# Performance work log

Hardware: AMD Instinct MI355X
Metric: run time of the kernel (lower is better)

The kernel has to match this reference:

```python
import jax, jax.numpy as jnp
import numpy as np

N = 20000      # nodes
E = 320000     # edges
DIN = 128
DOUT = 10
H = 1024
HM = 256
EPS = 1e-5


def setup_inputs() -> dict:
    key = jax.random.key(0)
    ks = jax.random.split(key, 16)
    sc = 0.02
    return {
        "x": jax.random.normal(ks[0], (N, DIN), dtype=jnp.float32),
        "edge_index": jax.random.randint(ks[1], (2, E), 0, N, dtype=jnp.int64),
        "edge_weight": jax.random.uniform(ks[2], (E,), dtype=jnp.float32),
        "W1": jax.random.normal(ks[3], (DIN, H), dtype=jnp.float32) * sc,
        "b1": jnp.zeros((H,), jnp.float32),
        "g1": jnp.ones((H,), jnp.float32),
        "beta1": jnp.zeros((H,), jnp.float32),
        "W2": jax.random.normal(ks[4], (H, H), dtype=jnp.float32) * sc,
        "b2": jnp.zeros((H,), jnp.float32),
        "g2": jnp.ones((H,), jnp.float32),
        "beta2": jnp.zeros((H,), jnp.float32),
        "Wl1": jax.random.normal(ks[5], (H, HM), dtype=jnp.float32) * sc,
        "bl1": jnp.zeros((HM,), jnp.float32),
        "Wl2": jax.random.normal(ks[6], (HM, DOUT), dtype=jnp.float32) * sc,
        "bl2": jnp.zeros((DOUT,), jnp.float32),
    }


def _gcn_conv(x, W, b, src, dst, w):
    # PyG GCNConv: linear transform, symmetric normalization (self-loops
    # already appended to src/dst/w), scatter-add aggregation at dst.
    h = x @ W                                        # [N, out]
    deg = jax.ops.segment_sum(w, dst, num_segments=N)
    dinv = jnp.where(deg > 0, jax.lax.rsqrt(deg), 0.0)
    norm = dinv[src] * w * dinv[dst]                 # [E+N]
    agg = jax.ops.segment_sum(norm[:, None] * h[src], dst, num_segments=N)
    return agg + b


def _batchnorm(x, g, b):
    m = x.mean(axis=0)
    v = jnp.mean(jnp.square(x - m), axis=0)          # biased var (torch BN)
    return g * (x - m) * jax.lax.rsqrt(v + EPS) + b


def reference(x, edge_index, edge_weight,
              W1, b1, g1, beta1, W2, b2, g2, beta2,
              Wl1, bl1, Wl2, bl2):
    loop = jnp.arange(N, dtype=edge_index.dtype)
    src = jnp.concatenate([edge_index[0], loop])
    dst = jnp.concatenate([edge_index[1], loop])
    w = jnp.concatenate([edge_weight, jnp.ones((N,), edge_weight.dtype)])

    h = jax.nn.relu(_batchnorm(_gcn_conv(x, W1, b1, src, dst, w), g1, beta1))
    h = jax.nn.relu(_batchnorm(_gcn_conv(h, W2, b2, src, dst, w), g2, beta2))
    h = jax.nn.relu(h @ Wl1 + bl1) @ Wl2 + bl2
    return jax.nn.log_softmax(h, axis=1)
```

## Files before the change

### kernel.cpp

```cpp
#include <hip/hip_runtime.h>
#include <math.h>

static constexpr int Nn  = 20000;
static constexpr int Ne  = 320000;
static constexpr int DIN = 128;
static constexpr int DOUTc = 10;
static constexpr int Hc  = 1024;
static constexpr int HMc = 256;
static constexpr float EPSc = 1e-5f;
static constexpr int NB_SCAN = (Nn + 255) / 256;

typedef __bf16 bf16_t;
typedef __bf16 bf16x8 __attribute__((ext_vector_type(8)));
typedef __bf16 bf16x4 __attribute__((ext_vector_type(4)));
typedef float  f32x4  __attribute__((ext_vector_type(4)));

__device__ __forceinline__ void gload_lds16(const bf16_t* g, bf16_t* lds) {
    __builtin_amdgcn_global_load_lds(
        (const __attribute__((address_space(1))) void*)g,
        (__attribute__((address_space(3))) void*)lds, 16, 0, 0);
}

__global__ __launch_bounds__(256)
void deg_init_k(float* __restrict__ deg, int* __restrict__ cnt, float* __restrict__ stats)
{
    int i = blockIdx.x * 256 + threadIdx.x;
    if (i < Nn) { deg[i] = 1.0f; cnt[i] = 0; }
    if (i < 4 * Hc) stats[i] = 0.f;
}

__global__ __launch_bounds__(256)
void deg_edge_k(const float* __restrict__ w, const int* __restrict__ dstv,
                float* __restrict__ deg, int* __restrict__ cnt) {
    int e = blockIdx.x * 256 + threadIdx.x;
    if (e < Ne) {
        int d = dstv[e];
        atomicAdd(&deg[d], w[e]);
        atomicAdd(&cnt[d], 1);
    }
}

__global__ __launch_bounds__(256)
void scanA_k(const int* __restrict__ cnt, int* __restrict__ row_ptr, int* __restrict__ blk,
             float* __restrict__ deg)
{
    __shared__ int wsum[4];
    int b = blockIdx.x, tid = threadIdx.x, lane = tid & 63, wv = tid >> 6;
    int i = b * 256 + tid;
    if (i < Nn) deg[i] = rsqrtf(deg[i]);
    int v = (i < Nn) ? cnt[i] : 0;
    int s = v;
    #pragma unroll
    for (int off = 1; off < 64; off <<= 1) {
        int t = __shfl_up(s, off, 64);
        if (lane >= off) s += t;
    }
    if (lane == 63) wsum[wv] = s;
    __syncthreads();
    int wo = 0;
    #pragma unroll
    for (int k = 0; k < 4; ++k) if (k < wv) wo += wsum[k];
    if (i < Nn) row_ptr[i] = wo + s - v;
    if (tid == 255) blk[b] = wo + s;
}

__global__ __launch_bounds__(128)
void scanB_k(int* __restrict__ blk)
{
    __shared__ int w0;
    int tid = threadIdx.x, lane = tid & 63, wv = tid >> 6;
    int v = (tid < NB_SCAN) ? blk[tid] : 0;
    int s = v;
    #pragma unroll
    for (int off = 1; off < 64; off <<= 1) {
        int t = __shfl_up(s, off, 64);
        if (lane >= off) s += t;
    }
    if (tid == 63) w0 = s;
    __syncthreads();
    int excl = s - v + (wv ? w0 : 0);
    if (tid < NB_SCAN) blk[tid] = excl;
}

__global__ __launch_bounds__(256)
void scanC_k(int* __restrict__ row_ptr, const int* __restrict__ blk, int* __restrict__ cursor)
{
    int b = blockIdx.x;
    int i = b * 256 + threadIdx.x;
    if (i < Nn) {
        int r = row_ptr[i] + blk[b];
        row_ptr[i] = r;
        cursor[i]  = r;
    }
    if (i == 0) row_ptr[Nn] = Ne;
}

__global__ __launch_bounds__(256)
void csr_fill_k(const int* __restrict__ srcv, const int* __restrict__ dstv,
                const float* __restrict__ w, const float* __restrict__ dinv,
                int* __restrict__ cursor, int* __restrict__ csr_src,
                float* __restrict__ csr_coeff)
{
    int e = blockIdx.x * 256 + threadIdx.x;
    if (e >= Ne) return;
    int s = srcv[e], d = dstv[e];
    int pos = atomicAdd(&cursor[d], 1);
    csr_src[pos]   = s;
    csr_coeff[pos] = dinv[s] * w[e] * dinv[d];
}

__global__ __launch_bounds__(256)
void spmm_x_k(const bf16x8* __restrict__ x8, const int* __restrict__ row_ptr,
              const int* __restrict__ csr_src, const float* __restrict__ csr_coeff,
              const float* __restrict__ dinv, bf16x8* __restrict__ out8)
{
    int panel = blockIdx.x & 3;
    int node  = (blockIdx.x >> 2) * 64 + (threadIdx.x >> 2);
    if (node >= Nn) return;
    int f = (threadIdx.x & 3) + panel * 4;
    float c = dinv[node]; c = c * c;
    bf16x8 hv = x8[(size_t)node * 16 + f];
    float acc[8];
    #pragma unroll
    for (int i = 0; i < 8; ++i) acc[i] = c * (float)hv[i];
    int beg = row_ptr[node], end = row_ptr[node + 1];
    int j = beg;
    for (; j + 4 <= end; j += 4) {
        int   s0 = csr_src[j + 0], s1 = csr_src[j + 1];
        int   s2 = csr_src[j + 2], s3 = csr_src[j + 3];
        float c0 = csr_coeff[j + 0], c1 = csr_coeff[j + 1];
        float c2 = csr_coeff[j + 2], c3 = csr_coeff[j + 3];
        bf16x8 v0 = x8[(size_t)s0 * 16 + f];
        bf16x8 v1 = x8[(size_t)s1 * 16 + f];
        bf16x8 v2 = x8[(size_t)s2 * 16 + f];
        bf16x8 v3 = x8[(size_t)s3 * 16 + f];
        #pragma unroll
        for (int i = 0; i < 8; ++i) {
            acc[i] = fmaf(c0, (float)v0[i], acc[i]);
            acc[i] = fmaf(c1, (float)v1[i], acc[i]);
            acc[i] = fmaf(c2, (float)v2[i], acc[i]);
            acc[i] = fmaf(c3, (float)v3[i], acc[i]);
        }
    }
    for (; j < end; ++j) {
        int   s  = csr_src[j];
        float cf = csr_coeff[j];
        bf16x8 v = x8[(size_t)s * 16 + f];
        #pragma unroll
        for (int i = 0; i < 8; ++i) acc[i] = fmaf(cf, (float)v[i], acc[i]);
    }
    bf16x8 o;
    #pragma unroll
    for (int i = 0; i < 8; ++i) o[i] = (bf16_t)acc[i];
    out8[(size_t)node * 16 + f] = o;
}

__global__ __launch_bounds__(256)
void spmm_h_k(const bf16x8* __restrict__ h8, const int* __restrict__ row_ptr,
              const int* __restrict__ csr_src, const float* __restrict__ csr_coeff,
              const float* __restrict__ dinv, bf16x8* __restrict__ out8)
{
    int panel = blockIdx.x & 7;
    int node  = (blockIdx.x >> 3) * 16 + (threadIdx.x >> 4);
    int f     = (threadIdx.x & 15) + panel * 16;
    float c = dinv[node]; c = c * c;
    bf16x8 hv = h8[(size_t)node * 128 + f];
    float acc[8];
    #pragma unroll
    for (int i = 0; i < 8; ++i) acc[i] = c * (float)hv[i];
    int beg = row_ptr[node], end = row_ptr[node + 1];
    int j = beg;
    for (; j + 4 <= end; j += 4) {
        int   s0 = csr_src[j + 0], s1 = csr_src[j + 1];
        int   s2 = csr_src[j + 2], s3 = csr_src[j + 3];
        float c0 = csr_coeff[j + 0], c1 = csr_coeff[j + 1];
        float c2 = csr_coeff[j + 2], c3 = csr_coeff[j + 3];
        bf16x8 v0 = h8[(size_t)s0 * 128 + f];
        bf16x8 v1 = h8[(size_t)s1 * 128 + f];
        bf16x8 v2 = h8[(size_t)s2 * 128 + f];
        bf16x8 v3 = h8[(size_t)s3 * 128 + f];
        #pragma unroll
        for (int i = 0; i < 8; ++i) {
            acc[i] = fmaf(c0, (float)v0[i], acc[i]);
            acc[i] = fmaf(c1, (float)v1[i], acc[i]);
            acc[i] = fmaf(c2, (float)v2[i], acc[i]);
            acc[i] = fmaf(c3, (float)v3[i], acc[i]);
        }
    }
    for (; j < end; ++j) {
        int   s  = csr_src[j];
        float cf = csr_coeff[j];
        bf16x8 v = h8[(size_t)s * 128 + f];
        #pragma unroll
        for (int i = 0; i < 8; ++i) acc[i] = fmaf(cf, (float)v[i], acc[i]);
    }
    bf16x8 o;
    #pragma unroll
    for (int i = 0; i < 8; ++i) o[i] = (bf16_t)acc[i];
    out8[(size_t)node * 128 + f] = o;
}

template<int RK, int CN>
__global__ __launch_bounds__(256)
void transpose_bf16_k(const float* __restrict__ W, bf16_t* __restrict__ Wt)
{
    __shared__ float tile[32][33];
    int bx = blockIdx.x * 32;
    int by = blockIdx.y * 32;
    int tx = threadIdx.x & 31, ty = threadIdx.x >> 5;
    #pragma unroll
    for (int p = 0; p < 32; p += 8)
        tile[ty + p][tx] = W[(size_t)(by + ty + p) * CN + bx + tx];
    __syncthreads();
    #pragma unroll
    for (int p = 0; p < 32; p += 8)
        Wt[(size_t)(bx + ty + p) * RK + by + tx] = (bf16_t)tile[tx][ty + p];
}

__global__ __launch_bounds__(256)
void cvt_bf16_k(const float4* __restrict__ in, bf16x4* __restrict__ out, int n4)
{
    int i = blockIdx.x * 256 + threadIdx.x;
    if (i >= n4) return;
    float4 v = in[i];
    bf16x4 o = { (bf16_t)v.x, (bf16_t)v.y, (bf16_t)v.z, (bf16_t)v.w };
    out[i] = o;
}

template<int NC, int KD, bool BIAS, bool RELU, bool OUTBF, bool STATS>
__global__ __launch_bounds__(256)
void gemm_bf16_k(const bf16_t* __restrict__ A, const bf16_t* __restrict__ Bt,
                 const float* __restrict__ bias, void* __restrict__ Cv, int M,
                 float* __restrict__ s1g, float* __restrict__ s2g)
{
    __shared__ __align__(16) bf16_t Asm[128 * 32];
    __shared__ __align__(16) bf16_t Bsm[128 * 32];
    const int tid  = threadIdx.x;
    const int w    = tid >> 6;
    const int lane = tid & 63;
    const int bm = blockIdx.y * 128, bn = blockIdx.x * 128;
    const int l15 = lane & 15, quad = lane >> 4;
    const int wm = (w & 1) * 64, wn = (w >> 1) * 64;
    const int swz = quad ^ ((l15 >> 1) & 3);

    const int srow = lane >> 2;
    const int scol = 8 * ((lane & 3) ^ ((lane >> 3) & 3));
    const int c0 = w * 32;
    int ga0 = bm + c0 + srow;       if (ga0 >= M) ga0 = M - 1;
    int ga1 = bm + c0 + 16 + srow;  if (ga1 >= M) ga1 = M - 1;
    const bf16_t* gA0 = A + (size_t)ga0 * KD + scol;
    const bf16_t* gA1 = A + (size_t)ga1 * KD + scol;
    const bf16_t* gB0 = Bt + (size_t)(bn + c0 + srow) * KD + scol;
    const bf16_t* gB1 = gB0 + (size_t)16 * KD;
    bf16_t* lA0 = Asm + (c0 +  0) * 32;
    bf16_t* lA1 = Asm + (c0 + 16) * 32;
    bf16_t* lB0 = Bsm + (c0 +  0) * 32;
    bf16_t* lB1 = Bsm + (c0 + 16) * 32;

    const bf16_t* pA = Asm + (wm + l15) * 32 + swz * 8;
    const bf16_t* pB = Bsm + (wn + l15) * 32 + swz * 8;

    f32x4 acc[4][4] = {};

    for (int k0 = 0; k0 < KD; k0 += 32) {
        gload_lds16(gA0 + k0, lA0);
        gload_lds16(gA1 + k0, lA1);
        gload_lds16(gB0 + k0, lB0);
        gload_lds16(gB1 + k0, lB1);
        __syncthreads();
        bf16x8 af[4], bfr[4];
        #pragma unroll
        for (int t = 0; t < 4; ++t) {
            af[t]  = *(const bf16x8*)(pA + t * 16 * 32);
            bfr[t] = *(const bf16x8*)(pB + t * 16 * 32);
        }
        #pragma unroll
        for (int mt = 0; mt < 4; ++mt)
            #pragma unroll
            for (int nt = 0; nt < 4; ++nt)
                acc[mt][nt] = __builtin_amdgcn_mfma_f32_16x16x32_bf16(
                    af[mt], bfr[nt], acc[mt][nt], 0, 0, 0);
        __syncthreads();
    }

    #pragma unroll
    for (int mt = 0; mt < 4; ++mt) {
        #pragma unroll
        for (int r = 0; r < 4; ++r) {
            int row = bm + wm + mt * 16 + quad * 4 + r;
            if (row >= M) continue;
            #pragma unroll
            for (int nt = 0; nt < 4; ++nt) {
                int col = bn + wn + nt * 16 + l15;
                float v = acc[mt][nt][r];
                if (BIAS) v += bias[col];
                if (RELU) v = fmaxf(v, 0.f);
                if (OUTBF) ((bf16_t*)Cv)[(size_t)row * NC + col] = (bf16_t)v;
                else       ((float*)Cv)[(size_t)row * NC + col] = v;
            }
        }
    }

    if (STATS) {
        #pragma unroll
        for (int nt = 0; nt < 4; ++nt) {
            float ps = 0.f, pq = 0.f;
            #pragma unroll
            for (int mt = 0; mt < 4; ++mt)
                #pragma unroll
                for (int r = 0; r < 4; ++r) {
                    int row = bm + wm + mt * 16 + quad * 4 + r;
                    if (row < M) {
                        float v = acc[mt][nt][r];
                        ps += v;
                        pq = fmaf(v, v, pq);
                    }
                }
            ps += __shfl_down(ps, 32, 64); ps += __shfl_down(ps, 16, 64);
            pq += __shfl_down(pq, 32, 64); pq += __shfl_down(pq, 16, 64);
            if (quad == 0) {
                int col = bn + wn + nt * 16 + l15;
                atomicAdd(&s1g[col], ps);
                atomicAdd(&s2g[col], pq);
            }
        }
    }
}

__global__ __launch_bounds__(256)
void bn_stats_k(const bf16_t* __restrict__ x, float* __restrict__ s1, float* __restrict__ s2)
{
    int c = blockIdx.x * 256 + threadIdx.x;
    int r0 = blockIdx.y * 250;
    float s = 0.f, q = 0.f;
    const bf16_t* p = x + (size_t)r0 * Hc + c;
    for (int r = 0; r < 250; ++r) {
        float v = (float)p[(size_t)r * Hc];
        s += v;
        q = fmaf(v, v, q);
    }
    atomicAdd(&s1[c], s);
    atomicAdd(&s2[c], q);
}

__global__ __launch_bounds__(256)
void bn_apply_k(const bf16x8* __restrict__ x8, const float* __restrict__ s1,
                const float* __restrict__ s2, const float* __restrict__ g,
                const float* __restrict__ beta, bf16x8* __restrict__ out8)
{
    int idx = blockIdx.x * 256 + threadIdx.x;
    int c8 = (idx & 127) << 3;
    bf16x8 v = x8[idx];
    bf16x8 o;
    #pragma unroll
    for (int i = 0; i < 8; ++i) {
        int c = c8 + i;
        float mean = s1[c] * (1.0f / Nn);
        float var  = s2[c] * (1.0f / Nn) - mean * mean;
        float sc = g[c] * rsqrtf(var + EPSc);
        float sh = beta[c] - mean * sc;
        o[i] = (bf16_t)fmaxf(fmaf((float)v[i], sc, sh), 0.f);
    }
    out8[idx] = o;
}

__global__ __launch_bounds__(256)
void head_k(const float* __restrict__ z, const float* __restrict__ Wl2,
            const float* __restrict__ bl2, float* __restrict__ out)
{
    int wave = threadIdx.x >> 6;
    int lane = threadIdx.x & 63;
    int node = blockIdx.x * 4 + wave;
    const float4 zv = *(const float4*)(z + (size_t)node * HMc + lane * 4);
    float p[DOUTc];
    #pragma unroll
    for (int j = 0; j < DOUTc; ++j) p[j] = 0.f;
    const float zz[4] = {zv.x, zv.y, zv.z, zv.w};
    #pragma unroll
    for (int i = 0; i < 4; ++i) {
        int k = lane * 4 + i;
        const float* wrow = Wl2 + (size_t)k * DOUTc;
        #pragma unroll
        for (int j = 0; j < DOUTc; ++j) p[j] = fmaf(zz[i], wrow[j], p[j]);
    }
    #pragma unroll
    for (int j = 0; j < DOUTc; ++j) {
        #pragma unroll
        for (int off = 32; off > 0; off >>= 1) p[j] += __shfl_down(p[j], off, 64);
    }
    if (lane == 0) {
        float v[DOUTc];
        float m = -1e30f;
        #pragma unroll
        for (int j = 0; j < DOUTc; ++j) { v[j] = p[j] + bl2[j]; m = fmaxf(m, v[j]); }
        float s = 0.f;
        #pragma unroll
        for (int j = 0; j < DOUTc; ++j) s += expf(v[j] - m);
        float ls = logf(s) + m;
        #pragma unroll
        for (int j = 0; j < DOUTc; ++j) out[(size_t)node * DOUTc + j] = v[j] - ls;
    }
}

extern "C" void kernel_launch(void* const* d_in, const int* in_sizes, int n_in,
                              void* d_out, int out_size, void* d_ws, size_t ws_size,
                              hipStream_t stream)
{
    (void)in_sizes; (void)n_in; (void)out_size; (void)ws_size;
    const float* x    = (const float*)d_in[0];
    const int*   ei   = (const int*)d_in[1];
    const float* ew   = (const float*)d_in[2];
    const float* W1   = (const float*)d_in[3];
    const float* gam1 = (const float*)d_in[5];
    const float* bet1 = (const float*)d_in[6];
    const float* W2   = (const float*)d_in[7];
    const float* gam2 = (const float*)d_in[9];
    const float* bet2 = (const float*)d_in[10];
    const float* Wl1  = (const float*)d_in[11];
    const float* bl1  = (const float*)d_in[12];
    const float* Wl2  = (const float*)d_in[13];
    const float* bl2  = (const float*)d_in[14];
    float* out = (float*)d_out;

    float* zhead = (float*)d_ws;
    float* dinv  = zhead + (size_t)Nn * HMc;
    float* stats = dinv + Nn;
    float* s1a = stats, *s2a = stats + Hc, *s1b = stats + 2 * Hc, *s2b = stats + 3 * Hc;
    int*   cnt      = (int*)(stats + 4 * Hc);
    int*   row_ptr  = cnt + Nn;
    int*   cursor   = row_ptr + Nn + 16;
    int*   blk      = cursor + Nn;
    int*   csr_src  = blk + 128;
    float* csr_coef = (float*)(csr_src + Ne);
    bf16_t* xb   = (bf16_t*)(csr_coef + Ne);
    bf16_t* xagg = xb + (size_t)Nn * DIN;
    bf16_t* hgem = xagg + (size_t)Nn * DIN;
    bf16_t* hbf  = hgem + (size_t)Nn * Hc;
    bf16_t* W1t  = hbf + (size_t)Nn * Hc;
    bf16_t* W2t  = W1t + (size_t)Hc * DIN;
    bf16_t* Wl1t = W2t + (size_t)Hc * Hc;

    const int* srcv = ei;
    const int* dstv = ei + Ne;

    deg_init_k<<<NB_SCAN, 256, 0, stream>>>(dinv, cnt, stats);
    deg_edge_k<<<(Ne + 255) / 256, 256, 0, stream>>>(ew, dstv, dinv, cnt);
    scanA_k<<<NB_SCAN, 256, 0, stream>>>(cnt, row_ptr, blk, dinv);
    scanB_k<<<1, 128, 0, stream>>>(blk);
    scanC_k<<<NB_SCAN, 256, 0, stream>>>(row_ptr, blk, cursor);
    csr_fill_k<<<(Ne + 255) / 256, 256, 0, stream>>>(srcv, dstv, ew, dinv, cursor,
                                                     csr_src, csr_coef);
    transpose_bf16_k<DIN, Hc><<<dim3(Hc / 32, DIN / 32), 256, 0, stream>>>(W1, W1t);
    transpose_bf16_k<Hc, Hc><<<dim3(Hc / 32, Hc / 32), 256, 0, stream>>>(W2, W2t);
    transpose_bf16_k<Hc, HMc><<<dim3(HMc / 32, Hc / 32), 256, 0, stream>>>(Wl1, Wl1t);
    cvt_bf16_k<<<(Nn * DIN / 4 + 255) / 256, 256, 0, stream>>>(
        (const float4*)x, (bf16x4*)xb, Nn * DIN / 4);

    const int MB = (Nn + 127) / 128;

    spmm_x_k<<<4 * ((Nn + 63) / 64), 256, 0, stream>>>(
        (const bf16x8*)xb, row_ptr, csr_src, csr_coef, dinv, (bf16x8*)xagg);
    gemm_bf16_k<Hc, DIN, false, false, true, true><<<dim3(Hc / 128, MB), 256, 0, stream>>>(
        xagg, W1t, nullptr, hgem, Nn, s1a, s2a);
    bn_apply_k<<<Nn * Hc / 8 / 256, 256, 0, stream>>>(
        (const bf16x8*)hgem, s1a, s2a, gam1, bet1, (bf16x8*)hbf);

    gemm_bf16_k<Hc, Hc, false, false, true, false><<<dim3(Hc / 128, MB), 256, 0, stream>>>(
        hbf, W2t, nullptr, hgem, Nn, nullptr, nullptr);
    spmm_h_k<<<8 * (Nn / 16), 256, 0, stream>>>(
        (const bf16x8*)hgem, row_ptr, csr_src, csr_coef, dinv, (bf16x8*)hbf);
    bn_stats_k<<<dim3(Hc / 256, 80), 256, 0, stream>>>(hbf, s1b, s2b);
    bn_apply_k<<<Nn * Hc / 8 / 256, 256, 0, stream>>>(
        (const bf16x8*)hbf, s1b, s2b, gam2, bet2, (bf16x8*)hgem);

    gemm_bf16_k<HMc, Hc, true, true, false, false><<<dim3(HMc / 128, MB), 256, 0, stream>>>(
        hgem, Wl1t, bl1, zhead, Nn, nullptr, nullptr);
    head_k<<<Nn / 4, 256, 0, stream>>>(zhead, Wl2, bl2, out);
}
```

Before: 439.2 us.

## Fuse BN2 statistics into SpMM, merge weight transposes, store head activations in bf16

Layer-2 batchnorm sum and sum-of-squares are now reduced inside the aggregation kernel with shuffles, shared memory and atomics, so the separate bn_stats pass over the 20000x1024 activation is removed. The edge loop gains an 8-way unrolled gather to keep more loads in flight. The three weight transposes become one launch, and the MLP hidden output is written in bf16 rather than fp32, which halves that traffic. In exchange there are more atomics per block, statistics are taken from fp32 accumulators instead of the bf16-rounded values, and the head now reads bf16 inputs.

```diff
diff --git a/kernel.cpp b/kernel.cpp
--- a/kernel.cpp
+++ b/kernel.cpp
@@ -158,11 +158,15 @@
 __global__ __launch_bounds__(256)
 void spmm_h_k(const bf16x8* __restrict__ h8, const int* __restrict__ row_ptr,
               const int* __restrict__ csr_src, const float* __restrict__ csr_coeff,
-              const float* __restrict__ dinv, bf16x8* __restrict__ out8)
-{
+              const float* __restrict__ dinv, bf16x8* __restrict__ out8,
+              float* __restrict__ s1g, float* __restrict__ s2g)
+{
+    __shared__ float smS[4][16][8];
+    __shared__ float smQ[4][16][8];
     int panel = blockIdx.x & 7;
     int node  = (blockIdx.x >> 3) * 16 + (threadIdx.x >> 4);
-    int f     = (threadIdx.x & 15) + panel * 16;
+    int fu    = threadIdx.x & 15;
+    int f     = fu + panel * 16;
     float c = dinv[node]; c = c * c;
     bf16x8 hv = h8[(size_t)node * 128 + f];
     float acc[8];
@@ -170,6 +174,35 @@
     for (int i = 0; i < 8; ++i) acc[i] = c * (float)hv[i];
     int beg = row_ptr[node], end = row_ptr[node + 1];
     int j = beg;
+    for (; j + 8 <= end; j += 8) {
+        int   s0 = csr_src[j + 0], s1 = csr_src[j + 1];
+        int   s2 = csr_src[j + 2], s3 = csr_src[j + 3];
+        int   s4 = csr_src[j + 4], s5 = csr_src[j + 5];
+        int   s6 = csr_src[j + 6], s7 = csr_src[j + 7];
+        float c0 = csr_coeff[j + 0], c1 = csr_coeff[j + 1];
+        float c2 = csr_coeff[j + 2], c3 = csr_coeff[j + 3];
+        float c4 = csr_coeff[j + 4], c5 = csr_coeff[j + 5];
+        float c6 = csr_coeff[j + 6], c7 = csr_coeff[j + 7];
+        bf16x8 v0 = h8[(size_t)s0 * 128 + f];
+        bf16x8 v1 = h8[(size_t)s1 * 128 + f];
+        bf16x8 v2 = h8[(size_t)s2 * 128 + f];
+        bf16x8 v3 = h8[(size_t)s3 * 128 + f];
+        bf16x8 v4 = h8[(size_t)s4 * 128 + f];
+        bf16x8 v5 = h8[(size_t)s5 * 128 + f];
+        bf16x8 v6 = h8[(size_t)s6 * 128 + f];
+        bf16x8 v7 = h8[(size_t)s7 * 128 + f];
+        #pragma unroll
+        for (int i = 0; i < 8; ++i) {
+            acc[i] = fmaf(c0, (float)v0[i], acc[i]);
+            acc[i] = fmaf(c1, (float)v1[i], acc[i]);
+            acc[i] = fmaf(c2, (float)v2[i], acc[i]);
+            acc[i] = fmaf(c3, (float)v3[i], acc[i]);
+            acc[i] = fmaf(c4, (float)v4[i], acc[i]);
+            acc[i] = fmaf(c5, (float)v5[i], acc[i]);
+            acc[i] = fmaf(c6, (float)v6[i], acc[i]);
+            acc[i] = fmaf(c7, (float)v7[i], acc[i]);
+        }
+    }
     for (; j + 4 <= end; j += 4) {
         int   s0 = csr_src[j + 0], s1 = csr_src[j + 1];
         int   s2 = csr_src[j + 2], s3 = csr_src[j + 3];
@@ -198,23 +231,53 @@
     #pragma unroll
     for (int i = 0; i < 8; ++i) o[i] = (bf16_t)acc[i];
     out8[(size_t)node * 128 + f] = o;
-}
-
-template<int RK, int CN>
-__global__ __launch_bounds__(256)
-void transpose_bf16_k(const float* __restrict__ W, bf16_t* __restrict__ Wt)
+
+    int lane = threadIdx.x & 63, wv = threadIdx.x >> 6;
+    float ps[8], pq[8];
+    #pragma unroll
+    for (int i = 0; i < 8; ++i) { ps[i] = acc[i]; pq[i] = acc[i] * acc[i]; }
+    #pragma unroll
+    for (int i = 0; i < 8; ++i) {
+        ps[i] += __shfl_down(ps[i], 32, 64); ps[i] += __shfl_down(ps[i], 16, 64);
+        pq[i] += __shfl_down(pq[i], 32, 64); pq[i] += __shfl_down(pq[i], 16, 64);
+    }
+    if (lane < 16) {
+        #pragma unroll
+        for (int i = 0; i < 8; ++i) { smS[wv][lane][i] = ps[i]; smQ[wv][lane][i] = pq[i]; }
+    }
+    __syncthreads();
+    if (threadIdx.x < 16) {
+        int u = threadIdx.x;
+        #pragma unroll
+        for (int i = 0; i < 8; ++i) {
+            float a = smS[0][u][i] + smS[1][u][i] + smS[2][u][i] + smS[3][u][i];
+            float b = smQ[0][u][i] + smQ[1][u][i] + smQ[2][u][i] + smQ[3][u][i];
+            int col = (u + panel * 16) * 8 + i;
+            atomicAdd(&s1g[col], a);
+            atomicAdd(&s2g[col], b);
+        }
+    }
+}
+
+__global__ __launch_bounds__(256)
+void transpose_all_k(const float* __restrict__ W1, const float* __restrict__ W2,
+                     const float* __restrict__ Wl1, bf16_t* __restrict__ W1t,
+                     bf16_t* __restrict__ W2t, bf16_t* __restrict__ Wl1t)
 {
     __shared__ float tile[32][33];
-    int bx = blockIdx.x * 32;
-    int by = blockIdx.y * 32;
+    int b = blockIdx.x;
+    const float* W; bf16_t* Wt; int R, C, bx, by;
+    if (b < 128)       { W = W1;  Wt = W1t;  R = DIN; C = Hc;  int t = b;        bx = (t & 31) * 32; by = (t >> 5) * 32; }
+    else if (b < 1152) { W = W2;  Wt = W2t;  R = Hc;  C = Hc;  int t = b - 128;  bx = (t & 31) * 32; by = (t >> 5) * 32; }
+    else               { W = Wl1; Wt = Wl1t; R = Hc;  C = HMc; int t = b - 1152; bx = (t & 7) * 32;  by = (t >> 3) * 32; }
     int tx = threadIdx.x & 31, ty = threadIdx.x >> 5;
     #pragma unroll
     for (int p = 0; p < 32; p += 8)
-        tile[ty + p][tx] = W[(size_t)(by + ty + p) * CN + bx + tx];
+        tile[ty + p][tx] = W[(size_t)(by + ty + p) * C + bx + tx];
     __syncthreads();
     #pragma unroll
     for (int p = 0; p < 32; p += 8)
-        Wt[(size_t)(bx + ty + p) * RK + by + tx] = (bf16_t)tile[tx][ty + p];
+        Wt[(size_t)(bx + ty + p) * R + by + tx] = (bf16_t)tile[tx][ty + p];
 }
 
 __global__ __launch_bounds__(256)
@@ -328,22 +391,6 @@
 }
 
 __global__ __launch_bounds__(256)
-void bn_stats_k(const bf16_t* __restrict__ x, float* __restrict__ s1, float* __restrict__ s2)
-{
-    int c = blockIdx.x * 256 + threadIdx.x;
-    int r0 = blockIdx.y * 250;
-    float s = 0.f, q = 0.f;
-    const bf16_t* p = x + (size_t)r0 * Hc + c;
-    for (int r = 0; r < 250; ++r) {
-        float v = (float)p[(size_t)r * Hc];
-        s += v;
-        q = fmaf(v, v, q);
-    }
-    atomicAdd(&s1[c], s);
-    atomicAdd(&s2[c], q);
-}
-
-__global__ __launch_bounds__(256)
 void bn_apply_k(const bf16x8* __restrict__ x8, const float* __restrict__ s1,
                 const float* __restrict__ s2, const float* __restrict__ g,
                 const float* __restrict__ beta, bf16x8* __restrict__ out8)
@@ -365,17 +412,17 @@
 }
 
 __global__ __launch_bounds__(256)
-void head_k(const float* __restrict__ z, const float* __restrict__ Wl2,
+void head_k(const bf16_t* __restrict__ z, const float* __restrict__ Wl2,
             const float* __restrict__ bl2, float* __restrict__ out)
 {
     int wave = threadIdx.x >> 6;
     int lane = threadIdx.x & 63;
     int node = blockIdx.x * 4 + wave;
-    const float4 zv = *(const float4*)(z + (size_t)node * HMc + lane * 4);
+    const bf16x4 zv = *(const bf16x4*)(z + (size_t)node * HMc + lane * 4);
     float p[DOUTc];
     #pragma unroll
     for (int j = 0; j < DOUTc; ++j) p[j] = 0.f;
-    const float zz[4] = {zv.x, zv.y, zv.z, zv.w};
+    const float zz[4] = {(float)zv[0], (float)zv[1], (float)zv[2], (float)zv[3]};
     #pragma unroll
     for (int i = 0; i < 4; ++i) {
         int k = lane * 4 + i;
@@ -422,8 +469,7 @@
     const float* bl2  = (const float*)d_in[14];
     float* out = (float*)d_out;
 
-    float* zhead = (float*)d_ws;
-    float* dinv  = zhead + (size_t)Nn * HMc;
+    float* dinv  = (float*)d_ws;
     float* stats = dinv + Nn;
     float* s1a = stats, *s2a = stats + Hc, *s1b = stats + 2 * Hc, *s2b = stats + 3 * Hc;
     int*   cnt      = (int*)(stats + 4 * Hc);
@@ -432,13 +478,14 @@
     int*   blk      = cursor + Nn;
     int*   csr_src  = blk + 128;
     float* csr_coef = (float*)(csr_src + Ne);
-    bf16_t* xb   = (bf16_t*)(csr_coef + Ne);
-    bf16_t* xagg = xb + (size_t)Nn * DIN;
-    bf16_t* hgem = xagg + (size_t)Nn * DIN;
-    bf16_t* hbf  = hgem + (size_t)Nn * Hc;
-    bf16_t* W1t  = hbf + (size_t)Nn * Hc;
-    bf16_t* W2t  = W1t + (size_t)Hc * DIN;
-    bf16_t* Wl1t = W2t + (size_t)Hc * Hc;
+    bf16_t* xb    = (bf16_t*)(csr_coef + Ne);
+    bf16_t* xagg  = xb + (size_t)Nn * DIN;
+    bf16_t* hgem  = xagg + (size_t)Nn * DIN;
+    bf16_t* hbf   = hgem + (size_t)Nn * Hc;
+    bf16_t* zhead = hbf + (size_t)Nn * Hc;
+    bf16_t* W1t   = zhead + (size_t)Nn * HMc;
+    bf16_t* W2t   = W1t + (size_t)Hc * DIN;
+    bf16_t* Wl1t  = W2t + (size_t)Hc * Hc;
 
     const int* srcv = ei;
     const int* dstv = ei + Ne;
@@ -450,9 +497,7 @@
     scanC_k<<<NB_SCAN, 256, 0, stream>>>(row_ptr, blk, cursor);
     csr_fill_k<<<(Ne + 255) / 256, 256, 0, stream>>>(srcv, dstv, ew, dinv, cursor,
                                                      csr_src, csr_coef);
-    transpose_bf16_k<DIN, Hc><<<dim3(Hc / 32, DIN / 32), 256, 0, stream>>>(W1, W1t);
-    transpose_bf16_k<Hc, Hc><<<dim3(Hc / 32, Hc / 32), 256, 0, stream>>>(W2, W2t);
-    transpose_bf16_k<Hc, HMc><<<dim3(HMc / 32, Hc / 32), 256, 0, stream>>>(Wl1, Wl1t);
+    transpose_all_k<<<1408, 256, 0, stream>>>(W1, W2, Wl1, W1t, W2t, Wl1t);
     cvt_bf16_k<<<(Nn * DIN / 4 + 255) / 256, 256, 0, stream>>>(
         (const float4*)x, (bf16x4*)xb, Nn * DIN / 4);
 
@@ -468,12 +513,11 @@
     gemm_bf16_k<Hc, Hc, false, false, true, false><<<dim3(Hc / 128, MB), 256, 0, stream>>>(
         hbf, W2t, nullptr, hgem, Nn, nullptr, nullptr);
     spmm_h_k<<<8 * (Nn / 16), 256, 0, stream>>>(
-        (const bf16x8*)hgem, row_ptr, csr_src, csr_coef, dinv, (bf16x8*)hbf);
-    bn_stats_k<<<dim3(Hc / 256, 80), 256, 0, stream>>>(hbf, s1b, s2b);
+        (const bf16x8*)hgem, row_ptr, csr_src, csr_coef, dinv, (bf16x8*)hbf, s1b, s2b);
     bn_apply_k<<<Nn * Hc / 8 / 256, 256, 0, stream>>>(
         (const bf16x8*)hbf, s1b, s2b, gam2, bet2, (bf16x8*)hgem);
 
-    gemm_bf16_k<HMc, Hc, true, true, false, false><<<dim3(HMc / 128, MB), 256, 0, stream>>>(
+    gemm_bf16_k<HMc, Hc, true, true, true, false><<<dim3(HMc / 128, MB), 256, 0, stream>>>(
         hgem, Wl1t, bl1, zhead, Nn, nullptr, nullptr);
     head_k<<<Nn / 4, 256, 0, stream>>>(zhead, Wl2, bl2, out);
 }
```

After: 599.3 us. 1.36x slower.
